# Kernel tuning notes

Hardware: AMD Instinct MI355X
Metric: run time of the kernel (lower is better)

Reference implementation:

```python
import jax, jax.numpy as jnp
import numpy as np
import math

B, S, H = 4, 4096, 64
WINDOW = 2


def setup_inputs() -> dict:
    key = jax.random.key(0)
    ks = jax.random.split(key, 7)
    s = 0.05
    return {
        "feature": jax.random.normal(ks[0], (B, S, H), dtype=jnp.float32),
        "Wq": jax.random.normal(ks[1], (H, H), dtype=jnp.float32) * s,
        "bq": jax.random.normal(ks[2], (H,), dtype=jnp.float32) * s,
        "Wk": jax.random.normal(ks[3], (H, H), dtype=jnp.float32) * s,
        "bk": jax.random.normal(ks[4], (H,), dtype=jnp.float32) * s,
        "Wv": jax.random.normal(ks[5], (H, H), dtype=jnp.float32) * s,
        "bv": jax.random.normal(ks[6], (H,), dtype=jnp.float32) * s,
    }


def reference(feature, Wq, bq, Wk, bk, Wv, bv):
    b, seq, d_k = feature.shape
    # torch nn.Linear: y = x @ W.T + b
    q = feature @ Wq.T + bq  # [B,S,H]
    k = feature @ Wk.T + bk
    v = feature @ Wv.T + bv

    # banded 0/1 mask, |i-j| <= window, then softmax over the FULL row
    # (faithful to the original: zeros outside the band also get exp(0)=1 weight)
    idx = jnp.arange(seq)
    band = (jnp.abs(idx[:, None] - idx[None, :]) <= WINDOW).astype(jnp.float32)  # [S,S]
    weights = jax.nn.softmax(band, axis=-1)  # [S,S]

    # locally-averaged K: weights @ k, shared across batch
    mixed_k = jnp.einsum('st,bth->bsh', weights, k)  # [B,S,H]
    scores = jnp.einsum('bsh,bth->bst', q, mixed_k) / math.sqrt(d_k)  # [B,S,S]
    attn = jax.nn.softmax(scores, axis=-1)
    out = jnp.einsum('bst,bth->bsh', attn, v)  # [B,S,H]
    return out
```

## Files before the change

### kernel.cpp

```cpp
#include <hip/hip_runtime.h>
#include <hip/hip_bf16.h>
#include <math.h>

#define SEQ 4096
#define HD  64
#define NBATCH 4

#define EM1   1.71828182845904523536f
#define INVD5 (1.0f/(4096.f + 5.f*EM1))
#define INVD4 (1.0f/(4096.f + 4.f*EM1))
#define INVD3 (1.0f/(4096.f + 3.f*EM1))

typedef __attribute__((ext_vector_type(8))) short short8;
typedef __attribute__((ext_vector_type(4))) short short4v;
typedef __attribute__((ext_vector_type(4))) float f32x4;

__device__ __forceinline__ f32x4 mfma16(short8 a, short8 b, f32x4 c) {
    return __builtin_amdgcn_mfma_f32_16x16x32_bf16(a, b, c, 0, 0, 0);
}

__device__ __forceinline__ short bfs(float x) {
    __hip_bfloat16 h = __float2bfloat16(x);
    return *(short*)&h;
}

__device__ __forceinline__ float sf(short s) {
    __hip_bfloat16 h;
    *(short*)&h = s;
    return __bfloat162float(h);
}

__device__ __forceinline__ short8 pack8(float4 a, float4 b) {
    short8 r;
    r[0] = bfs(a.x); r[1] = bfs(a.y); r[2] = bfs(a.z); r[3] = bfs(a.w);
    r[4] = bfs(b.x); r[5] = bfs(b.y); r[6] = bfs(b.z); r[7] = bfs(b.w);
    return r;
}

__device__ __forceinline__ float b2f(__hip_bfloat16 h) { return __bfloat162float(h); }

#define WSTR 72

__global__ __launch_bounds__(256, 2) void projm_kernel(
    const float* __restrict__ feat,
    const float* __restrict__ Wq, const float* __restrict__ Wk,
    const float* __restrict__ Wv,
    const float* __restrict__ bq, const float* __restrict__ bk,
    const float* __restrict__ bv,
    __hip_bfloat16* __restrict__ qsb, float* __restrict__ kpart,
    float* __restrict__ vpart, __hip_bfloat16* __restrict__ Mpart,
    float* __restrict__ kedge)
{
    __shared__ __hip_bfloat16 WbL[3 * 64 * WSTR];
    __shared__ __hip_bfloat16 kT[64 * 40];
    __shared__ __hip_bfloat16 vT[64 * 40];
    __shared__ __hip_bfloat16 lvt[64 * 40];
    __shared__ float kred[2][64];
    __shared__ float vred[2][64];

    const int tid  = threadIdx.x;
    const int wv   = tid >> 6, lane = tid & 63;
    const int rh   = wv & 1;
    const int grp  = wv >> 1;
    const int quad = lane >> 4, ln = lane & 15;
    const int R0 = blockIdx.x * 32;
    const int b  = R0 >> 12;
    const int t0 = R0 & (SEQ - 1);
    const int chunk = blockIdx.x & 127;

    short8 af0, af1;
    {
        const float* fp = feat + (size_t)(R0 + rh * 16 + ln) * HD + quad * 8;
        af0 = pack8(*(const float4*)(fp),      *(const float4*)(fp + 4));
        af1 = pack8(*(const float4*)(fp + 32), *(const float4*)(fp + 36));
    }

    short8 hf0, hf1;
    const bool hflag = (rh == 0) ? (t0 > 0) : (t0 < SEQ - 32);
    if (grp == 1) {
        const int hrow = (rh == 0) ? (t0 - 2 + ln) : (t0 + 32 + ln);
        if (ln < 2 && hflag) {
            const float* fp = feat + ((size_t)(b << 12) + hrow) * HD + quad * 8;
            hf0 = pack8(*(const float4*)(fp),      *(const float4*)(fp + 4));
            hf1 = pack8(*(const float4*)(fp + 32), *(const float4*)(fp + 36));
        } else {
            #pragma unroll
            for (int j = 0; j < 8; ++j) { hf0[j] = 0; hf1[j] = 0; }
        }
    }

    {
        const int r = tid >> 2, c = (tid & 3) * 16;
        #pragma unroll
        for (int m = 0; m < 3; ++m) {
            const float* W = (m == 0) ? Wq : (m == 1) ? Wk : Wv;
            const float s = (m == 0) ? 0.125f : 1.f;
            const float* src = W + r * 64 + c;
            float4 a0 = *(const float4*)(src);
            float4 a1 = *(const float4*)(src + 4);
            float4 a2 = *(const float4*)(src + 8);
            float4 a3 = *(const float4*)(src + 12);
            a0.x*=s; a0.y*=s; a0.z*=s; a0.w*=s;
            a1.x*=s; a1.y*=s; a1.z*=s; a1.w*=s;
            a2.x*=s; a2.y*=s; a2.z*=s; a2.w*=s;
            a3.x*=s; a3.y*=s; a3.z*=s; a3.w*=s;
            __hip_bfloat16* dst = WbL + m * 64 * WSTR + r * WSTR + c;
            *(short8*)(dst)     = pack8(a0, a1);
            *(short8*)(dst + 8) = pack8(a2, a3);
        }
    }
    __syncthreads();

    if (grp == 0) {
        #pragma unroll
        for (int ct = 0; ct < 4; ++ct) {
            const int col = ct * 16 + ln;
            {
                const __hip_bfloat16* wp = WbL + col * WSTR + quad * 8;
                short8 b0 = *(const short8*)(wp);
                short8 b1 = *(const short8*)(wp + 32);
                f32x4 c = {};
                c = mfma16(af0, b0, c);
                c = mfma16(af1, b1, c);
                const float bl = bq[col] * 0.125f;
                #pragma unroll
                for (int rr = 0; rr < 4; ++rr)
                    qsb[(size_t)(R0 + rh * 16 + quad * 4 + rr) * HD + col] =
                        __float2bfloat16(c[rr] + bl);
            }
            {
                const __hip_bfloat16* wp = WbL + 64 * WSTR + col * WSTR + quad * 8;
                short8 b0 = *(const short8*)(wp);
                short8 b1 = *(const short8*)(wp + 32);
                f32x4 c = {};
                c = mfma16(af0, b0, c);
                c = mfma16(af1, b1, c);
                float tot = c[0] + c[1] + c[2] + c[3];
                tot += __shfl_xor(tot, 16);
                tot += __shfl_xor(tot, 32);
                if (quad == 0) kred[rh][col] = tot;
                const float bl = bk[col];
                #pragma unroll
                for (int rr = 0; rr < 4; ++rr)
                    kT[col * 40 + rh * 16 + quad * 4 + rr] =
                        __float2bfloat16(c[rr] + bl);
            }
        }
    } else {
        #pragma unroll
        for (int ct = 0; ct < 4; ++ct) {
            const int col = ct * 16 + ln;
            const __hip_bfloat16* wp = WbL + 2 * 64 * WSTR + col * WSTR + quad * 8;
            short8 b0 = *(const short8*)(wp);
            short8 b1 = *(const short8*)(wp + 32);
            f32x4 c = {};
            c = mfma16(af0, b0, c);
            c = mfma16(af1, b1, c);
            float tot = c[0] + c[1] + c[2] + c[3];
            tot += __shfl_xor(tot, 16);
            tot += __shfl_xor(tot, 32);
            if (quad == 0) vred[rh][col] = tot;
            const float bl = bv[col];
            #pragma unroll
            for (int rr = 0; rr < 4; ++rr)
                vT[col * 40 + 2 + rh * 16 + quad * 4 + rr] =
                    __float2bfloat16(c[rr] + bl);
            f32x4 hc = {};
            hc = mfma16(hf0, b0, hc);
            hc = mfma16(hf1, b1, hc);
            if (quad == 0) {
                const int base = (rh == 0) ? 0 : 34;
                vT[col * 40 + base]     = __float2bfloat16(hflag ? hc[0] + bl : 0.f);
                vT[col * 40 + base + 1] = __float2bfloat16(hflag ? hc[1] + bl : 0.f);
            }
        }
    }
    __syncthreads();

    if (tid < 64) {
        kpart[(size_t)blockIdx.x * 64 + tid] =
            kred[0][tid] + kred[1][tid] + 32.f * bk[tid];
        vpart[(size_t)blockIdx.x * 64 + tid] =
            vred[0][tid] + vred[1][tid] + 32.f * bv[tid];
    }

    {
        const int h = tid & 63;
        const int tb = (tid >> 6) * 8;
        short4v u0 = *(const short4v*)&vT[h * 40 + tb];
        short4v u1 = *(const short4v*)&vT[h * 40 + tb + 4];
        short4v u2 = *(const short4v*)&vT[h * 40 + tb + 8];
        float w[12];
        #pragma unroll
        for (int j = 0; j < 4; ++j) {
            w[j]     = sf(u0[j]);
            w[j + 4] = sf(u1[j]);
            w[j + 8] = sf(u2[j]);
        }
        #pragma unroll
        for (int i = 0; i < 8; ++i)
            lvt[h * 40 + tb + i] =
                __float2bfloat16(w[i] + w[i+1] + w[i+2] + w[i+3] + w[i+4]);
    }

    if (chunk == 0) {
        const int t = tid >> 6, h = tid & 63;
        kedge[b * 512 + t * 64 + h] = b2f(kT[h * 40 + t]);
    } else if (chunk == 127) {
        const int t = tid >> 6, h = tid & 63;
        kedge[b * 512 + (4 + t) * 64 + h] = b2f(kT[h * 40 + 28 + t]);
    }
    __syncthreads();

    __hip_bfloat16* mp = Mpart + (size_t)(b * 128 + chunk) * 4096;
    {
        short8 a = *(const short8*)&kT[(wv * 16 + ln) * 40 + quad * 8];
        #pragma unroll
        for (int ct = 0; ct < 4; ++ct) {
            short8 bb = *(const short8*)&lvt[(ct * 16 + ln) * 40 + quad * 8];
            f32x4 acc = {};
            acc = mfma16(a, bb, acc);
            #pragma unroll
            for (int rr = 0; rr < 4; ++rr)
                mp[(wv * 16 + quad * 4 + rr) * 64 + ct * 16 + ln] =
                    __float2bfloat16(acc[rr]);
        }
    }
}

__global__ __launch_bounds__(256) void redprep_kernel(
    const __hip_bfloat16* __restrict__ Mpart, const float* __restrict__ kpart,
    const float* __restrict__ vpart, const float* __restrict__ kedge,
    __hip_bfloat16* __restrict__ MTm, float* __restrict__ mktotF,
    float* __restrict__ ktotF, float* __restrict__ VDs,
    float* __restrict__ VtotF)
{
    const int b = blockIdx.y, x = blockIdx.x;
    const int tid = threadIdx.x;

    if (x < 32) {
        __shared__ float part[16][132];
        const int gl = tid >> 4;
        const int s  = tid & 15;
        const int e  = x * 128 + gl * 8;
        const __hip_bfloat16* src =
            Mpart + ((size_t)b * 128 + s * 8) * 4096 + e;
        float sum[8] = {0.f,0.f,0.f,0.f,0.f,0.f,0.f,0.f};
        #pragma unroll
        for (int c = 0; c < 8; ++c) {
            short8 v = *(const short8*)(src + (size_t)c * 4096);
            #pragma unroll
            for (int j = 0; j < 8; ++j) sum[j] += sf(v[j]);
        }
        #pragma unroll
        for (int j = 0; j < 8; ++j) part[s][gl * 8 + j] = sum[j];
        __syncthreads();
        if (tid < 128) {
            float t = 0.f;
            #pragma unroll
            for (int ss = 0; ss < 16; ++ss) t += part[ss][tid];
            const int e2 = x * 128 + tid;
            const int h1 = e2 >> 6, h2 = e2 & 63;
            MTm[(size_t)b * 4096 + h2 * 64 + h1] =
                __float2bfloat16((EM1 * INVD5) * t);
        }
        return;
    }

    __shared__ float red[4][64];
    __shared__ float red2[4][64];
    const int g = tid >> 6, h2 = tid & 63;
    {
        float kp = 0.f, vp = 0.f;
        for (int j = 0; j < 32; ++j) {
            kp += kpart[(size_t)(b * 128 + g * 32 + j) * 64 + h2];
            vp += vpart[(size_t)(b * 128 + g * 32 + j) * 64 + h2];
        }
        red[g][h2] = kp;
        red2[g][h2] = vp;
    }
    __syncthreads();
    if (tid < 64) {
        const int hh = tid;
        const float kt = red[0][hh] + red[1][hh] + red[2][hh] + red[3][hh];
        const float vt = red2[0][hh] + red2[1][hh] + red2[2][hh] + red2[3][hh];
        const float e0 = kedge[b * 512 + 0 * 64 + hh];
        const float e1 = kedge[b * 512 + 1 * 64 + hh];
        const float e2 = kedge[b * 512 + 2 * 64 + hh];
        const float e3 = kedge[b * 512 + 3 * 64 + hh];
        const float f0 = kedge[b * 512 + 4 * 64 + hh];
        const float f1 = kedge[b * 512 + 5 * 64 + hh];
        const float f2 = kedge[b * 512 + 6 * 64 + hh];
        const float f3 = kedge[b * 512 + 7 * 64 + hh];
        const float Sint = 5.f*kt - 4.f*e0 - 3.f*e1 - 2.f*e2 - e3
                         - f0 - 2.f*f1 - 3.f*f2 - 4.f*f3;
        const float SlocD = Sint * INVD5
                          + (e0+e1+e2 + f1+f2+f3) * INVD3
                          + (e0+e1+e2+e3 + f0+f1+f2+f3) * INVD4;
        mktotF[b * 64 + hh] = kt * (4092.f*INVD5 + 2.f*INVD4 + 2.f*INVD3) + EM1 * SlocD;
        ktotF[b * 64 + hh]  = kt;
        VDs[b * 64 + hh]    = INVD5 * vt;
        VtotF[b * 64 + hh]  = vt;
    }
}

__global__ __launch_bounds__(128) void out_kernel(
    const __hip_bfloat16* __restrict__ qsb, const __hip_bfloat16* __restrict__ MTm,
    const float* __restrict__ mktotF, const float* __restrict__ ktotF,
    const float* __restrict__ VDs, const float* __restrict__ VtotF,
    float* __restrict__ out)
{
    const int tid = threadIdx.x;
    const int wv = tid >> 6, lane = tid & 63;
    const int quad = lane >> 4, ln = lane & 15;
    const int R0 = blockIdx.x * 16;
    const int b = R0 >> 12;

    short8 qa0, qa1;
    {
        const __hip_bfloat16* qp = qsb + (size_t)(R0 + ln) * HD + quad * 8;
        qa0 = *(const short8*)qp;
        qa1 = *(const short8*)(qp + 32);
    }

    const __hip_bfloat16* mtb = MTm + (size_t)b * 4096;
    f32x4 acc[2];
    #pragma unroll
    for (int i = 0; i < 2; ++i) {
        const int ct = wv * 2 + i;
        short8 b0 = *(const short8*)(mtb + (ct * 16 + ln) * 64 + quad * 8);
        short8 b1 = *(const short8*)(mtb + (ct * 16 + ln) * 64 + 32 + quad * 8);
        f32x4 c = {};
        c = mfma16(qa0, b0, c);
        c = mfma16(qa1, b1, c);
        acc[i] = c;
    }

    short8 mk0, mk1, kt0, kt1;
    #pragma unroll
    for (int j = 0; j < 8; ++j) {
        mk0[j] = bfs(mktotF[b * 64 + quad * 8 + j]);
        mk1[j] = bfs(mktotF[b * 64 + 32 + quad * 8 + j]);
        kt0[j] = bfs(ktotF[b * 64 + quad * 8 + j]);
        kt1[j] = bfs(ktotF[b * 64 + 32 + quad * 8 + j]);
    }
    f32x4 accd = {}, acck = {};
    accd = mfma16(qa0, mk0, accd);
    accd = mfma16(qa1, mk1, accd);
    acck = mfma16(qa0, kt0, acck);
    acck = mfma16(qa1, kt1, acck);

    float vt[2], vd[2];
    #pragma unroll
    for (int i = 0; i < 2; ++i) {
        const int ct = wv * 2 + i;
        vt[i] = VtotF[b * 64 + ct * 16 + ln];
        vd[i] = VDs[b * 64 + ct * 16 + ln];
    }

    float inv[4];
    #pragma unroll
    for (int r = 0; r < 4; ++r) inv[r] = 1.f / (4096.f + accd[r]);

    #pragma unroll
    for (int i = 0; i < 2; ++i)
        #pragma unroll
        for (int r = 0; r < 4; ++r)
            out[(size_t)(R0 + quad * 4 + r) * HD + (wv * 2 + i) * 16 + ln] =
                (vt[i] + acc[i][r] + acck[r] * vd[i]) * inv[r];
}

extern "C" void kernel_launch(void* const* d_in, const int* in_sizes, int n_in,
                              void* d_out, int out_size, void* d_ws, size_t ws_size,
                              hipStream_t stream)
{
    const float* feat = (const float*)d_in[0];
    const float* Wq = (const float*)d_in[1];
    const float* bq = (const float*)d_in[2];
    const float* Wk = (const float*)d_in[3];
    const float* bk = (const float*)d_in[4];
    const float* Wv = (const float*)d_in[5];
    const float* bv = (const float*)d_in[6];
    float* out = (float*)d_out;

    char* ws = (char*)d_ws;
    __hip_bfloat16* qsb    = (__hip_bfloat16*)(ws + 0);
    __hip_bfloat16* Mpart  = (__hip_bfloat16*)(ws + (2u << 20));
    float*          kpart  = (float*)(ws + (6u << 20));
    float*          vpart  = (float*)(ws + (6u << 20) + 131072);
    float*          kedge  = (float*)(ws + (6u << 20) + 262144);
    __hip_bfloat16* MTm    = (__hip_bfloat16*)(ws + (6u << 20) + 270336);
    float*          mktotF = (float*)(ws + (6u << 20) + 303104);
    float*          ktotF  = (float*)(ws + (6u << 20) + 304128);
    float*          VDs    = (float*)(ws + (6u << 20) + 305152);
    float*          VtotF  = (float*)(ws + (6u << 20) + 306176);

    projm_kernel<<<dim3(512), dim3(256), 0, stream>>>(
        feat, Wq, Wk, Wv, bq, bk, bv, qsb, kpart, vpart, Mpart, kedge);
    redprep_kernel<<<dim3(33, NBATCH), dim3(256), 0, stream>>>(
        Mpart, kpart, vpart, kedge, MTm, mktotF, ktotF, VDs, VtotF);
    out_kernel<<<dim3(1024), dim3(128), 0, stream>>>(
        qsb, MTm, mktotF, ktotF, VDs, VtotF, out);
}
```

Measured before the change: 79.43 us.

## Fuse three kernels into one cooperative kernel with grid-wide syncs

Merges the projection, reduction/prep and output kernels into one cooperative launch of 512 blocks separated by two grid.sync barriers. The goal is to remove two kernel launch gaps and inter-kernel drain and ramp time. The reduction is redistributed across all 512 blocks, and the output stage now covers 32 rows per block. The trade-off is grid-barrier cost and the requirement that all 512 blocks be co-resident, which the launch bounds of 2 blocks per CU should permit.

```diff
diff --git a/kernel.cpp b/kernel.cpp
--- a/kernel.cpp
+++ b/kernel.cpp
@@ -1,6 +1,9 @@
 #include <hip/hip_runtime.h>
 #include <hip/hip_bf16.h>
+#include <hip/hip_cooperative_groups.h>
 #include <math.h>
+
+namespace cg = cooperative_groups;
 
 #define SEQ 4096
 #define HD  64
@@ -41,7 +44,7 @@
 
 #define WSTR 72
 
-__global__ __launch_bounds__(256, 2) void projm_kernel(
+__global__ __launch_bounds__(256, 2) void fused_kernel(
     const float* __restrict__ feat,
     const float* __restrict__ Wq, const float* __restrict__ Wk,
     const float* __restrict__ Wv,
@@ -49,7 +52,10 @@
     const float* __restrict__ bv,
     __hip_bfloat16* __restrict__ qsb, float* __restrict__ kpart,
     float* __restrict__ vpart, __hip_bfloat16* __restrict__ Mpart,
-    float* __restrict__ kedge)
+    float* __restrict__ kedge,
+    __hip_bfloat16* __restrict__ MTm, float* __restrict__ mktotF,
+    float* __restrict__ ktotF, float* __restrict__ VDs,
+    float* __restrict__ VtotF, float* __restrict__ out)
 {
     __shared__ __hip_bfloat16 WbL[3 * 64 * WSTR];
     __shared__ __hip_bfloat16 kT[64 * 40];
@@ -57,6 +63,11 @@
     __shared__ __hip_bfloat16 lvt[64 * 40];
     __shared__ float kred[2][64];
     __shared__ float vred[2][64];
+    __shared__ float part[8][33];
+    __shared__ float red[4][64];
+    __shared__ float red2[4][64];
+
+    cg::grid_group grid = cg::this_grid();
 
     const int tid  = threadIdx.x;
     const int wv   = tid >> 6, lane = tid & 63;
@@ -212,8 +223,8 @@
     }
     __syncthreads();
 
-    __hip_bfloat16* mp = Mpart + (size_t)(b * 128 + chunk) * 4096;
-    {
+    {
+        __hip_bfloat16* mp = Mpart + (size_t)(b * 128 + chunk) * 4096;
         short8 a = *(const short8*)&kT[(wv * 16 + ln) * 40 + quad * 8];
         #pragma unroll
         for (int ct = 0; ct < 4; ++ct) {
@@ -226,148 +237,136 @@
                     __float2bfloat16(acc[rr]);
         }
     }
-}
-
-__global__ __launch_bounds__(256) void redprep_kernel(
-    const __hip_bfloat16* __restrict__ Mpart, const float* __restrict__ kpart,
-    const float* __restrict__ vpart, const float* __restrict__ kedge,
-    __hip_bfloat16* __restrict__ MTm, float* __restrict__ mktotF,
-    float* __restrict__ ktotF, float* __restrict__ VDs,
-    float* __restrict__ VtotF)
-{
-    const int b = blockIdx.y, x = blockIdx.x;
-    const int tid = threadIdx.x;
-
-    if (x < 32) {
-        __shared__ float part[16][132];
-        const int gl = tid >> 4;
-        const int s  = tid & 15;
-        const int e  = x * 128 + gl * 8;
-        const __hip_bfloat16* src =
-            Mpart + ((size_t)b * 128 + s * 8) * 4096 + e;
-        float sum[8] = {0.f,0.f,0.f,0.f,0.f,0.f,0.f,0.f};
-        #pragma unroll
-        for (int c = 0; c < 8; ++c) {
-            short8 v = *(const short8*)(src + (size_t)c * 4096);
+
+    __threadfence();
+    grid.sync();
+
+    {
+        const int bid = blockIdx.x;
+        if (bid < 4) {
+            const int bb = bid;
+            const int g = tid >> 6, hh = tid & 63;
+            float kp = 0.f, vp = 0.f;
+            for (int j = 0; j < 32; ++j) {
+                kp += kpart[(size_t)(bb * 128 + g * 32 + j) * 64 + hh];
+                vp += vpart[(size_t)(bb * 128 + g * 32 + j) * 64 + hh];
+            }
+            red[g][hh] = kp;
+            red2[g][hh] = vp;
+            __syncthreads();
+            if (tid < 64) {
+                const int h = tid;
+                const float kt = red[0][h] + red[1][h] + red[2][h] + red[3][h];
+                const float vt = red2[0][h] + red2[1][h] + red2[2][h] + red2[3][h];
+                const float e0 = kedge[bb * 512 + 0 * 64 + h];
+                const float e1 = kedge[bb * 512 + 1 * 64 + h];
+                const float e2 = kedge[bb * 512 + 2 * 64 + h];
+                const float e3 = kedge[bb * 512 + 3 * 64 + h];
+                const float f0 = kedge[bb * 512 + 4 * 64 + h];
+                const float f1 = kedge[bb * 512 + 5 * 64 + h];
+                const float f2 = kedge[bb * 512 + 6 * 64 + h];
+                const float f3 = kedge[bb * 512 + 7 * 64 + h];
+                const float Sint = 5.f*kt - 4.f*e0 - 3.f*e1 - 2.f*e2 - e3
+                                 - f0 - 2.f*f1 - 3.f*f2 - 4.f*f3;
+                const float SlocD = Sint * INVD5
+                                  + (e0+e1+e2 + f1+f2+f3) * INVD3
+                                  + (e0+e1+e2+e3 + f0+f1+f2+f3) * INVD4;
+                mktotF[bb * 64 + h] = kt * (4092.f*INVD5 + 2.f*INVD4 + 2.f*INVD3)
+                                    + EM1 * SlocD;
+                ktotF[bb * 64 + h]  = kt;
+                VDs[bb * 64 + h]    = INVD5 * vt;
+                VtotF[bb * 64 + h]  = vt;
+            }
+            __syncthreads();
+        }
+        {
+            const int bb = bid & 3, x = bid >> 2;
+            const int g = tid >> 5, e = tid & 31;
+            const int E = x * 32 + e;
+            const __hip_bfloat16* src =
+                Mpart + ((size_t)bb * 128 + g * 16) * 4096 + E;
+            float s = 0.f;
             #pragma unroll
-            for (int j = 0; j < 8; ++j) sum[j] += sf(v[j]);
-        }
-        #pragma unroll
-        for (int j = 0; j < 8; ++j) part[s][gl * 8 + j] = sum[j];
-        __syncthreads();
-        if (tid < 128) {
-            float t = 0.f;
+            for (int c = 0; c < 16; ++c) s += b2f(src[(size_t)c * 4096]);
+            part[g][e] = s;
+            __syncthreads();
+            if (tid < 32) {
+                float t = 0.f;
+                #pragma unroll
+                for (int g2 = 0; g2 < 8; ++g2) t += part[g2][tid];
+                const int E2 = x * 32 + tid;
+                const int h1 = E2 >> 6, h2 = E2 & 63;
+                MTm[(size_t)bb * 4096 + h2 * 64 + h1] =
+                    __float2bfloat16((EM1 * INVD5) * t);
+            }
+        }
+    }
+
+    __threadfence();
+    grid.sync();
+
+    {
+        const int sub = tid >> 7;
+        const int t2  = tid & 127;
+        const int w3  = t2 >> 6;
+        const int l3  = t2 & 63;
+        const int q3  = l3 >> 4, n3 = l3 & 15;
+        const int R0o = blockIdx.x * 32 + sub * 16;
+        const int b3  = R0o >> 12;
+
+        short8 qa0, qa1;
+        {
+            const __hip_bfloat16* qp = qsb + (size_t)(R0o + n3) * HD + q3 * 8;
+            qa0 = *(const short8*)qp;
+            qa1 = *(const short8*)(qp + 32);
+        }
+
+        const __hip_bfloat16* mtb = MTm + (size_t)b3 * 4096;
+        f32x4 acc[2];
+        #pragma unroll
+        for (int i = 0; i < 2; ++i) {
+            const int ct = w3 * 2 + i;
+            short8 b0 = *(const short8*)(mtb + (ct * 16 + n3) * 64 + q3 * 8);
+            short8 b1 = *(const short8*)(mtb + (ct * 16 + n3) * 64 + 32 + q3 * 8);
+            f32x4 c = {};
+            c = mfma16(qa0, b0, c);
+            c = mfma16(qa1, b1, c);
+            acc[i] = c;
+        }
+
+        short8 mk0, mk1, kt0, kt1;
+        #pragma unroll
+        for (int j = 0; j < 8; ++j) {
+            mk0[j] = bfs(mktotF[b3 * 64 + q3 * 8 + j]);
+            mk1[j] = bfs(mktotF[b3 * 64 + 32 + q3 * 8 + j]);
+            kt0[j] = bfs(ktotF[b3 * 64 + q3 * 8 + j]);
+            kt1[j] = bfs(ktotF[b3 * 64 + 32 + q3 * 8 + j]);
+        }
+        f32x4 accd = {}, acck = {};
+        accd = mfma16(qa0, mk0, accd);
+        accd = mfma16(qa1, mk1, accd);
+        acck = mfma16(qa0, kt0, acck);
+        acck = mfma16(qa1, kt1, acck);
+
+        float vt[2], vd[2];
+        #pragma unroll
+        for (int i = 0; i < 2; ++i) {
+            const int ct = w3 * 2 + i;
+            vt[i] = VtotF[b3 * 64 + ct * 16 + n3];
+            vd[i] = VDs[b3 * 64 + ct * 16 + n3];
+        }
+
+        float inv[4];
+        #pragma unroll
+        for (int r = 0; r < 4; ++r) inv[r] = 1.f / (4096.f + accd[r]);
+
+        #pragma unroll
+        for (int i = 0; i < 2; ++i)
             #pragma unroll
-            for (int ss = 0; ss < 16; ++ss) t += part[ss][tid];
-            const int e2 = x * 128 + tid;
-            const int h1 = e2 >> 6, h2 = e2 & 63;
-            MTm[(size_t)b * 4096 + h2 * 64 + h1] =
-                __float2bfloat16((EM1 * INVD5) * t);
-        }
-        return;
-    }
-
-    __shared__ float red[4][64];
-    __shared__ float red2[4][64];
-    const int g = tid >> 6, h2 = tid & 63;
-    {
-        float kp = 0.f, vp = 0.f;
-        for (int j = 0; j < 32; ++j) {
-            kp += kpart[(size_t)(b * 128 + g * 32 + j) * 64 + h2];
-            vp += vpart[(size_t)(b * 128 + g * 32 + j) * 64 + h2];
-        }
-        red[g][h2] = kp;
-        red2[g][h2] = vp;
-    }
-    __syncthreads();
-    if (tid < 64) {
-        const int hh = tid;
-        const float kt = red[0][hh] + red[1][hh] + red[2][hh] + red[3][hh];
-        const float vt = red2[0][hh] + red2[1][hh] + red2[2][hh] + red2[3][hh];
-        const float e0 = kedge[b * 512 + 0 * 64 + hh];
-        const float e1 = kedge[b * 512 + 1 * 64 + hh];
-        const float e2 = kedge[b * 512 + 2 * 64 + hh];
-        const float e3 = kedge[b * 512 + 3 * 64 + hh];
-        const float f0 = kedge[b * 512 + 4 * 64 + hh];
-        const float f1 = kedge[b * 512 + 5 * 64 + hh];
-        const float f2 = kedge[b * 512 + 6 * 64 + hh];
-        const float f3 = kedge[b * 512 + 7 * 64 + hh];
-        const float Sint = 5.f*kt - 4.f*e0 - 3.f*e1 - 2.f*e2 - e3
-                         - f0 - 2.f*f1 - 3.f*f2 - 4.f*f3;
-        const float SlocD = Sint * INVD5
-                          + (e0+e1+e2 + f1+f2+f3) * INVD3
-                          + (e0+e1+e2+e3 + f0+f1+f2+f3) * INVD4;
-        mktotF[b * 64 + hh] = kt * (4092.f*INVD5 + 2.f*INVD4 + 2.f*INVD3) + EM1 * SlocD;
-        ktotF[b * 64 + hh]  = kt;
-        VDs[b * 64 + hh]    = INVD5 * vt;
-        VtotF[b * 64 + hh]  = vt;
-    }
-}
-
-__global__ __launch_bounds__(128) void out_kernel(
-    const __hip_bfloat16* __restrict__ qsb, const __hip_bfloat16* __restrict__ MTm,
-    const float* __restrict__ mktotF, const float* __restrict__ ktotF,
-    const float* __restrict__ VDs, const float* __restrict__ VtotF,
-    float* __restrict__ out)
-{
-    const int tid = threadIdx.x;
-    const int wv = tid >> 6, lane = tid & 63;
-    const int quad = lane >> 4, ln = lane & 15;
-    const int R0 = blockIdx.x * 16;
-    const int b = R0 >> 12;
-
-    short8 qa0, qa1;
-    {
-        const __hip_bfloat16* qp = qsb + (size_t)(R0 + ln) * HD + quad * 8;
-        qa0 = *(const short8*)qp;
-        qa1 = *(const short8*)(qp + 32);
-    }
-
-    const __hip_bfloat16* mtb = MTm + (size_t)b * 4096;
-    f32x4 acc[2];
-    #pragma unroll
-    for (int i = 0; i < 2; ++i) {
-        const int ct = wv * 2 + i;
-        short8 b0 = *(const short8*)(mtb + (ct * 16 + ln) * 64 + quad * 8);
-        short8 b1 = *(const short8*)(mtb + (ct * 16 + ln) * 64 + 32 + quad * 8);
-        f32x4 c = {};
-        c = mfma16(qa0, b0, c);
-        c = mfma16(qa1, b1, c);
-        acc[i] = c;
-    }
-
-    short8 mk0, mk1, kt0, kt1;
-    #pragma unroll
-    for (int j = 0; j < 8; ++j) {
-        mk0[j] = bfs(mktotF[b * 64 + quad * 8 + j]);
-        mk1[j] = bfs(mktotF[b * 64 + 32 + quad * 8 + j]);
-        kt0[j] = bfs(ktotF[b * 64 + quad * 8 + j]);
-        kt1[j] = bfs(ktotF[b * 64 + 32 + quad * 8 + j]);
-    }
-    f32x4 accd = {}, acck = {};
-    accd = mfma16(qa0, mk0, accd);
-    accd = mfma16(qa1, mk1, accd);
-    acck = mfma16(qa0, kt0, acck);
-    acck = mfma16(qa1, kt1, acck);
-
-    float vt[2], vd[2];
-    #pragma unroll
-    for (int i = 0; i < 2; ++i) {
-        const int ct = wv * 2 + i;
-        vt[i] = VtotF[b * 64 + ct * 16 + ln];
-        vd[i] = VDs[b * 64 + ct * 16 + ln];
-    }
-
-    float inv[4];
-    #pragma unroll
-    for (int r = 0; r < 4; ++r) inv[r] = 1.f / (4096.f + accd[r]);
-
-    #pragma unroll
-    for (int i = 0; i < 2; ++i)
-        #pragma unroll
-        for (int r = 0; r < 4; ++r)
-            out[(size_t)(R0 + quad * 4 + r) * HD + (wv * 2 + i) * 16 + ln] =
-                (vt[i] + acc[i][r] + acck[r] * vd[i]) * inv[r];
+            for (int r = 0; r < 4; ++r)
+                out[(size_t)(R0o + q3 * 4 + r) * HD + (w3 * 2 + i) * 16 + n3] =
+                    (vt[i] + acc[i][r] + acck[r] * vd[i]) * inv[r];
+    }
 }
 
 extern "C" void kernel_launch(void* const* d_in, const int* in_sizes, int n_in,
@@ -395,10 +394,13 @@
     float*          VDs    = (float*)(ws + (6u << 20) + 305152);
     float*          VtotF  = (float*)(ws + (6u << 20) + 306176);
 
-    projm_kernel<<<dim3(512), dim3(256), 0, stream>>>(
-        feat, Wq, Wk, Wv, bq, bk, bv, qsb, kpart, vpart, Mpart, kedge);
-    redprep_kernel<<<dim3(33, NBATCH), dim3(256), 0, stream>>>(
-        Mpart, kpart, vpart, kedge, MTm, mktotF, ktotF, VDs, VtotF);
-    out_kernel<<<dim3(1024), dim3(128), 0, stream>>>(
-        qsb, MTm, mktotF, ktotF, VDs, VtotF, out);
-}
+    void* kargs[] = {
+        (void*)&feat, (void*)&Wq, (void*)&Wk, (void*)&Wv,
+        (void*)&bq, (void*)&bk, (void*)&bv,
+        (void*)&qsb, (void*)&kpart, (void*)&vpart, (void*)&Mpart,
+        (void*)&kedge, (void*)&MTm, (void*)&mktotF, (void*)&ktotF,
+        (void*)&VDs, (void*)&VtotF, (void*)&out
+    };
+    hipLaunchCooperativeKernel((void*)fused_kernel, dim3(512), dim3(256),
+                               kargs, 0, stream);
+}
```

Result: slower. 284.6 us (+258.3%).

## Coalesce q and Mpart stores, widen reduction grid, precast totals to bf16

Applied to the files above, without the earlier changes.

Q projection results are staged in shared memory and written to global memory as 16-byte rows instead of scattered 2-byte stores. Mpart partial products are stored in MFMA fragment order as contiguous 8-byte vectors, and the reduction kernel undoes that permutation when it writes MTm. The reduction grid grows from 33 to 129 blocks per batch, with each block summing a smaller slice. The mk/kt totals are stored as bf16 so out_kernel loads them as vectors instead of converting scalar floats per lane. This trades extra index arithmetic and a small shared buffer for fewer, wider memory transactions and more parallelism in the reduction.

```diff
diff --git a/kernel.cpp b/kernel.cpp
--- a/kernel.cpp
+++ b/kernel.cpp
@@ -40,6 +40,7 @@
 __device__ __forceinline__ float b2f(__hip_bfloat16 h) { return __bfloat162float(h); }
 
 #define WSTR 72
+#define QSTR 72
 
 __global__ __launch_bounds__(256, 2) void projm_kernel(
     const float* __restrict__ feat,
@@ -55,6 +56,7 @@
     __shared__ __hip_bfloat16 kT[64 * 40];
     __shared__ __hip_bfloat16 vT[64 * 40];
     __shared__ __hip_bfloat16 lvt[64 * 40];
+    __shared__ __hip_bfloat16 qR[32 * QSTR];
     __shared__ float kred[2][64];
     __shared__ float vred[2][64];
 
@@ -125,7 +127,7 @@
                 const float bl = bq[col] * 0.125f;
                 #pragma unroll
                 for (int rr = 0; rr < 4; ++rr)
-                    qsb[(size_t)(R0 + rh * 16 + quad * 4 + rr) * HD + col] =
+                    qR[(rh * 16 + quad * 4 + rr) * QSTR + col] =
                         __float2bfloat16(c[rr] + bl);
             }
             {
@@ -177,6 +179,12 @@
     }
     __syncthreads();
 
+    {
+        const int row = tid >> 3, c8 = tid & 7;
+        short8 v = *(const short8*)&qR[row * QSTR + c8 * 8];
+        *(short8*)(qsb + (size_t)(R0 + row) * HD + c8 * 8) = v;
+    }
+
     if (tid < 64) {
         kpart[(size_t)blockIdx.x * 64 + tid] =
             kred[0][tid] + kred[1][tid] + 32.f * bk[tid];
@@ -212,18 +220,18 @@
     }
     __syncthreads();
 
-    __hip_bfloat16* mp = Mpart + (size_t)(b * 128 + chunk) * 4096;
-    {
+    {
+        short4v* mpv = (short4v*)(Mpart + (size_t)(b * 128 + chunk) * 4096);
         short8 a = *(const short8*)&kT[(wv * 16 + ln) * 40 + quad * 8];
         #pragma unroll
         for (int ct = 0; ct < 4; ++ct) {
             short8 bb = *(const short8*)&lvt[(ct * 16 + ln) * 40 + quad * 8];
             f32x4 acc = {};
             acc = mfma16(a, bb, acc);
-            #pragma unroll
-            for (int rr = 0; rr < 4; ++rr)
-                mp[(wv * 16 + quad * 4 + rr) * 64 + ct * 16 + ln] =
-                    __float2bfloat16(acc[rr]);
+            short4v pv;
+            pv[0] = bfs(acc[0]); pv[1] = bfs(acc[1]);
+            pv[2] = bfs(acc[2]); pv[3] = bfs(acc[3]);
+            mpv[(wv * 4 + ct) * 64 + lane] = pv;
         }
     }
 }
@@ -231,36 +239,39 @@
 __global__ __launch_bounds__(256) void redprep_kernel(
     const __hip_bfloat16* __restrict__ Mpart, const float* __restrict__ kpart,
     const float* __restrict__ vpart, const float* __restrict__ kedge,
-    __hip_bfloat16* __restrict__ MTm, float* __restrict__ mktotF,
-    float* __restrict__ ktotF, float* __restrict__ VDs,
-    float* __restrict__ VtotF)
+    __hip_bfloat16* __restrict__ MTm, float* __restrict__ VDs,
+    float* __restrict__ VtotF, __hip_bfloat16* __restrict__ mktotB,
+    __hip_bfloat16* __restrict__ ktotB)
 {
     const int b = blockIdx.y, x = blockIdx.x;
     const int tid = threadIdx.x;
 
-    if (x < 32) {
-        __shared__ float part[16][132];
-        const int gl = tid >> 4;
-        const int s  = tid & 15;
-        const int e  = x * 128 + gl * 8;
+    if (x < 128) {
+        __shared__ float part[32][33];
+        const int cg = tid >> 3;
+        const int eg = tid & 7;
         const __hip_bfloat16* src =
-            Mpart + ((size_t)b * 128 + s * 8) * 4096 + e;
-        float sum[8] = {0.f,0.f,0.f,0.f,0.f,0.f,0.f,0.f};
-        #pragma unroll
-        for (int c = 0; c < 8; ++c) {
-            short8 v = *(const short8*)(src + (size_t)c * 4096);
-            #pragma unroll
-            for (int j = 0; j < 8; ++j) sum[j] += sf(v[j]);
-        }
-        #pragma unroll
-        for (int j = 0; j < 8; ++j) part[s][gl * 8 + j] = sum[j];
+            Mpart + ((size_t)b * 128 + cg * 4) * 4096 + x * 32 + eg * 4;
+        float s0 = 0.f, s1 = 0.f, s2 = 0.f, s3 = 0.f;
+        #pragma unroll
+        for (int c = 0; c < 4; ++c) {
+            short4v v = *(const short4v*)(src + (size_t)c * 4096);
+            s0 += sf(v[0]); s1 += sf(v[1]); s2 += sf(v[2]); s3 += sf(v[3]);
+        }
+        part[cg][eg * 4 + 0] = s0;
+        part[cg][eg * 4 + 1] = s1;
+        part[cg][eg * 4 + 2] = s2;
+        part[cg][eg * 4 + 3] = s3;
         __syncthreads();
-        if (tid < 128) {
+        if (tid < 32) {
             float t = 0.f;
             #pragma unroll
-            for (int ss = 0; ss < 16; ++ss) t += part[ss][tid];
-            const int e2 = x * 128 + tid;
-            const int h1 = e2 >> 6, h2 = e2 & 63;
+            for (int g = 0; g < 32; ++g) t += part[g][tid];
+            const int E  = x * 32 + tid;
+            const int rr = E & 3, l = (E >> 2) & 63;
+            const int ct = (E >> 8) & 3, w = (E >> 10) & 3;
+            const int h1 = w * 16 + (l >> 4) * 4 + rr;
+            const int h2 = ct * 16 + (l & 15);
             MTm[(size_t)b * 4096 + h2 * 64 + h1] =
                 __float2bfloat16((EM1 * INVD5) * t);
         }
@@ -297,8 +308,9 @@
         const float SlocD = Sint * INVD5
                           + (e0+e1+e2 + f1+f2+f3) * INVD3
                           + (e0+e1+e2+e3 + f0+f1+f2+f3) * INVD4;
-        mktotF[b * 64 + hh] = kt * (4092.f*INVD5 + 2.f*INVD4 + 2.f*INVD3) + EM1 * SlocD;
-        ktotF[b * 64 + hh]  = kt;
+        const float mk = kt * (4092.f*INVD5 + 2.f*INVD4 + 2.f*INVD3) + EM1 * SlocD;
+        mktotB[b * 64 + hh] = __float2bfloat16(mk);
+        ktotB[b * 64 + hh]  = __float2bfloat16(kt);
         VDs[b * 64 + hh]    = INVD5 * vt;
         VtotF[b * 64 + hh]  = vt;
     }
@@ -306,7 +318,7 @@
 
 __global__ __launch_bounds__(128) void out_kernel(
     const __hip_bfloat16* __restrict__ qsb, const __hip_bfloat16* __restrict__ MTm,
-    const float* __restrict__ mktotF, const float* __restrict__ ktotF,
+    const __hip_bfloat16* __restrict__ mktotB, const __hip_bfloat16* __restrict__ ktotB,
     const float* __restrict__ VDs, const float* __restrict__ VtotF,
     float* __restrict__ out)
 {
@@ -336,14 +348,11 @@
         acc[i] = c;
     }
 
-    short8 mk0, mk1, kt0, kt1;
-    #pragma unroll
-    for (int j = 0; j < 8; ++j) {
-        mk0[j] = bfs(mktotF[b * 64 + quad * 8 + j]);
-        mk1[j] = bfs(mktotF[b * 64 + 32 + quad * 8 + j]);
-        kt0[j] = bfs(ktotF[b * 64 + quad * 8 + j]);
-        kt1[j] = bfs(ktotF[b * 64 + 32 + quad * 8 + j]);
-    }
+    short8 mk0 = *(const short8*)(mktotB + b * 64 + quad * 8);
+    short8 mk1 = *(const short8*)(mktotB + b * 64 + 32 + quad * 8);
+    short8 kt0 = *(const short8*)(ktotB + b * 64 + quad * 8);
+    short8 kt1 = *(const short8*)(ktotB + b * 64 + 32 + quad * 8);
+
     f32x4 accd = {}, acck = {};
     accd = mfma16(qa0, mk0, accd);
     accd = mfma16(qa1, mk1, accd);
@@ -390,15 +399,15 @@
     float*          vpart  = (float*)(ws + (6u << 20) + 131072);
     float*          kedge  = (float*)(ws + (6u << 20) + 262144);
     __hip_bfloat16* MTm    = (__hip_bfloat16*)(ws + (6u << 20) + 270336);
-    float*          mktotF = (float*)(ws + (6u << 20) + 303104);
-    float*          ktotF  = (float*)(ws + (6u << 20) + 304128);
-    float*          VDs    = (float*)(ws + (6u << 20) + 305152);
-    float*          VtotF  = (float*)(ws + (6u << 20) + 306176);
+    float*          VDs    = (float*)(ws + (6u << 20) + 303104);
+    float*          VtotF  = (float*)(ws + (6u << 20) + 304128);
+    __hip_bfloat16* mktotB = (__hip_bfloat16*)(ws + (6u << 20) + 305152);
+    __hip_bfloat16* ktotB  = (__hip_bfloat16*)(ws + (6u << 20) + 305664);
 
     projm_kernel<<<dim3(512), dim3(256), 0, stream>>>(
         feat, Wq, Wk, Wv, bq, bk, bv, qsb, kpart, vpart, Mpart, kedge);
-    redprep_kernel<<<dim3(33, NBATCH), dim3(256), 0, stream>>>(
-        Mpart, kpart, vpart, kedge, MTm, mktotF, ktotF, VDs, VtotF);
+    redprep_kernel<<<dim3(129, NBATCH), dim3(256), 0, stream>>>(
+        Mpart, kpart, vpart, kedge, MTm, VDs, VtotF, mktotB, ktotB);
     out_kernel<<<dim3(1024), dim3(128), 0, stream>>>(
-        qsb, MTm, mktotF, ktotF, VDs, VtotF, out);
-}
+        qsb, MTm, mktotB, ktotB, VDs, VtotF, out);
+}
```

New measurement: 81.43 us. 2.5% more time.

## Replace partial-sum buffers and reduction kernel with global float atomics

Applied to the files above, without the earlier changes.

The projection kernel now accumulates the per-chunk 64x64 K^T·localV products and the K/V column totals straight into per-batch fp32 buffers with unsafeAtomicAdd, instead of writing bf16 partials for a separate reduction kernel. The small per-batch prep (mk, kt, vd, vt) moves into the output kernel's prologue and is shared through LDS, and the output kernel scales and converts the fp32 M matrix to bf16 on load. This drops one kernel launch and about 4 MB of partial-buffer traffic. In exchange it adds a memset, heavy atomic contention (128 chunks per batch adding into the same 4096 floats), and redundant prep work in every output block.

```diff
diff --git a/kernel.cpp b/kernel.cpp
--- a/kernel.cpp
+++ b/kernel.cpp
@@ -34,6 +34,13 @@
     short8 r;
     r[0] = bfs(a.x); r[1] = bfs(a.y); r[2] = bfs(a.z); r[3] = bfs(a.w);
     r[4] = bfs(b.x); r[5] = bfs(b.y); r[6] = bfs(b.z); r[7] = bfs(b.w);
+    return r;
+}
+
+__device__ __forceinline__ short8 pack8s(float4 a, float4 b, float s) {
+    short8 r;
+    r[0] = bfs(a.x*s); r[1] = bfs(a.y*s); r[2] = bfs(a.z*s); r[3] = bfs(a.w*s);
+    r[4] = bfs(b.x*s); r[5] = bfs(b.y*s); r[6] = bfs(b.z*s); r[7] = bfs(b.w*s);
     return r;
 }
 
@@ -47,8 +54,8 @@
     const float* __restrict__ Wv,
     const float* __restrict__ bq, const float* __restrict__ bk,
     const float* __restrict__ bv,
-    __hip_bfloat16* __restrict__ qsb, float* __restrict__ kpart,
-    float* __restrict__ vpart, __hip_bfloat16* __restrict__ Mpart,
+    __hip_bfloat16* __restrict__ qsb, float* __restrict__ MTf,
+    float* __restrict__ ktotF, float* __restrict__ VtotF,
     float* __restrict__ kedge)
 {
     __shared__ __hip_bfloat16 WbL[3 * 64 * WSTR];
@@ -178,10 +185,10 @@
     __syncthreads();
 
     if (tid < 64) {
-        kpart[(size_t)blockIdx.x * 64 + tid] =
-            kred[0][tid] + kred[1][tid] + 32.f * bk[tid];
-        vpart[(size_t)blockIdx.x * 64 + tid] =
-            vred[0][tid] + vred[1][tid] + 32.f * bv[tid];
+        unsafeAtomicAdd(&ktotF[b * 64 + tid],
+                        kred[0][tid] + kred[1][tid] + 32.f * bk[tid]);
+        unsafeAtomicAdd(&VtotF[b * 64 + tid],
+                        vred[0][tid] + vred[1][tid] + 32.f * bv[tid]);
     }
 
     {
@@ -212,8 +219,8 @@
     }
     __syncthreads();
 
-    __hip_bfloat16* mp = Mpart + (size_t)(b * 128 + chunk) * 4096;
-    {
+    {
+        float* mt = MTf + (size_t)b * 4096;
         short8 a = *(const short8*)&kT[(wv * 16 + ln) * 40 + quad * 8];
         #pragma unroll
         for (int ct = 0; ct < 4; ++ct) {
@@ -222,68 +229,32 @@
             acc = mfma16(a, bb, acc);
             #pragma unroll
             for (int rr = 0; rr < 4; ++rr)
-                mp[(wv * 16 + quad * 4 + rr) * 64 + ct * 16 + ln] =
-                    __float2bfloat16(acc[rr]);
-        }
-    }
-}
-
-__global__ __launch_bounds__(256) void redprep_kernel(
-    const __hip_bfloat16* __restrict__ Mpart, const float* __restrict__ kpart,
-    const float* __restrict__ vpart, const float* __restrict__ kedge,
-    __hip_bfloat16* __restrict__ MTm, float* __restrict__ mktotF,
-    float* __restrict__ ktotF, float* __restrict__ VDs,
-    float* __restrict__ VtotF)
+                unsafeAtomicAdd(
+                    &mt[(ct * 16 + ln) * 64 + wv * 16 + quad * 4 + rr], acc[rr]);
+        }
+    }
+}
+
+__global__ __launch_bounds__(128) void out_kernel(
+    const __hip_bfloat16* __restrict__ qsb, const float* __restrict__ MTf,
+    const float* __restrict__ ktotF, const float* __restrict__ VtotF,
+    const float* __restrict__ kedge, float* __restrict__ out)
 {
-    const int b = blockIdx.y, x = blockIdx.x;
+    __shared__ __align__(16) __hip_bfloat16 mkB[64];
+    __shared__ __align__(16) __hip_bfloat16 ktB[64];
+    __shared__ float vdL[64];
+    __shared__ float vtL[64];
+
     const int tid = threadIdx.x;
-
-    if (x < 32) {
-        __shared__ float part[16][132];
-        const int gl = tid >> 4;
-        const int s  = tid & 15;
-        const int e  = x * 128 + gl * 8;
-        const __hip_bfloat16* src =
-            Mpart + ((size_t)b * 128 + s * 8) * 4096 + e;
-        float sum[8] = {0.f,0.f,0.f,0.f,0.f,0.f,0.f,0.f};
-        #pragma unroll
-        for (int c = 0; c < 8; ++c) {
-            short8 v = *(const short8*)(src + (size_t)c * 4096);
-            #pragma unroll
-            for (int j = 0; j < 8; ++j) sum[j] += sf(v[j]);
-        }
-        #pragma unroll
-        for (int j = 0; j < 8; ++j) part[s][gl * 8 + j] = sum[j];
-        __syncthreads();
-        if (tid < 128) {
-            float t = 0.f;
-            #pragma unroll
-            for (int ss = 0; ss < 16; ++ss) t += part[ss][tid];
-            const int e2 = x * 128 + tid;
-            const int h1 = e2 >> 6, h2 = e2 & 63;
-            MTm[(size_t)b * 4096 + h2 * 64 + h1] =
-                __float2bfloat16((EM1 * INVD5) * t);
-        }
-        return;
-    }
-
-    __shared__ float red[4][64];
-    __shared__ float red2[4][64];
-    const int g = tid >> 6, h2 = tid & 63;
-    {
-        float kp = 0.f, vp = 0.f;
-        for (int j = 0; j < 32; ++j) {
-            kp += kpart[(size_t)(b * 128 + g * 32 + j) * 64 + h2];
-            vp += vpart[(size_t)(b * 128 + g * 32 + j) * 64 + h2];
-        }
-        red[g][h2] = kp;
-        red2[g][h2] = vp;
-    }
-    __syncthreads();
+    const int wv = tid >> 6, lane = tid & 63;
+    const int quad = lane >> 4, ln = lane & 15;
+    const int R0 = blockIdx.x * 16;
+    const int b = R0 >> 12;
+
     if (tid < 64) {
         const int hh = tid;
-        const float kt = red[0][hh] + red[1][hh] + red[2][hh] + red[3][hh];
-        const float vt = red2[0][hh] + red2[1][hh] + red2[2][hh] + red2[3][hh];
+        const float kt = ktotF[b * 64 + hh];
+        const float vt = VtotF[b * 64 + hh];
         const float e0 = kedge[b * 512 + 0 * 64 + hh];
         const float e1 = kedge[b * 512 + 1 * 64 + hh];
         const float e2 = kedge[b * 512 + 2 * 64 + hh];
@@ -297,24 +268,12 @@
         const float SlocD = Sint * INVD5
                           + (e0+e1+e2 + f1+f2+f3) * INVD3
                           + (e0+e1+e2+e3 + f0+f1+f2+f3) * INVD4;
-        mktotF[b * 64 + hh] = kt * (4092.f*INVD5 + 2.f*INVD4 + 2.f*INVD3) + EM1 * SlocD;
-        ktotF[b * 64 + hh]  = kt;
-        VDs[b * 64 + hh]    = INVD5 * vt;
-        VtotF[b * 64 + hh]  = vt;
-    }
-}
-
-__global__ __launch_bounds__(128) void out_kernel(
-    const __hip_bfloat16* __restrict__ qsb, const __hip_bfloat16* __restrict__ MTm,
-    const float* __restrict__ mktotF, const float* __restrict__ ktotF,
-    const float* __restrict__ VDs, const float* __restrict__ VtotF,
-    float* __restrict__ out)
-{
-    const int tid = threadIdx.x;
-    const int wv = tid >> 6, lane = tid & 63;
-    const int quad = lane >> 4, ln = lane & 15;
-    const int R0 = blockIdx.x * 16;
-    const int b = R0 >> 12;
+        const float mk = kt * (4092.f*INVD5 + 2.f*INVD4 + 2.f*INVD3) + EM1 * SlocD;
+        mkB[hh] = __float2bfloat16(mk);
+        ktB[hh] = __float2bfloat16(kt);
+        vdL[hh] = INVD5 * vt;
+        vtL[hh] = vt;
+    }
 
     short8 qa0, qa1;
     {
@@ -323,27 +282,30 @@
         qa1 = *(const short8*)(qp + 32);
     }
 
-    const __hip_bfloat16* mtb = MTm + (size_t)b * 4096;
+    const float SC = EM1 * INVD5;
+    const float* mtb = MTf + (size_t)b * 4096;
     f32x4 acc[2];
     #pragma unroll
     for (int i = 0; i < 2; ++i) {
         const int ct = wv * 2 + i;
-        short8 b0 = *(const short8*)(mtb + (ct * 16 + ln) * 64 + quad * 8);
-        short8 b1 = *(const short8*)(mtb + (ct * 16 + ln) * 64 + 32 + quad * 8);
+        const float* mrow = mtb + (ct * 16 + ln) * 64;
+        short8 b0 = pack8s(*(const float4*)(mrow + quad * 8),
+                           *(const float4*)(mrow + quad * 8 + 4), SC);
+        short8 b1 = pack8s(*(const float4*)(mrow + 32 + quad * 8),
+                           *(const float4*)(mrow + 36 + quad * 8), SC);
         f32x4 c = {};
         c = mfma16(qa0, b0, c);
         c = mfma16(qa1, b1, c);
         acc[i] = c;
     }
 
-    short8 mk0, mk1, kt0, kt1;
-    #pragma unroll
-    for (int j = 0; j < 8; ++j) {
-        mk0[j] = bfs(mktotF[b * 64 + quad * 8 + j]);
-        mk1[j] = bfs(mktotF[b * 64 + 32 + quad * 8 + j]);
-        kt0[j] = bfs(ktotF[b * 64 + quad * 8 + j]);
-        kt1[j] = bfs(ktotF[b * 64 + 32 + quad * 8 + j]);
-    }
+    __syncthreads();
+
+    short8 mk0 = *(const short8*)&mkB[quad * 8];
+    short8 mk1 = *(const short8*)&mkB[32 + quad * 8];
+    short8 kt0 = *(const short8*)&ktB[quad * 8];
+    short8 kt1 = *(const short8*)&ktB[32 + quad * 8];
+
     f32x4 accd = {}, acck = {};
     accd = mfma16(qa0, mk0, accd);
     accd = mfma16(qa1, mk1, accd);
@@ -354,8 +316,8 @@
     #pragma unroll
     for (int i = 0; i < 2; ++i) {
         const int ct = wv * 2 + i;
-        vt[i] = VtotF[b * 64 + ct * 16 + ln];
-        vd[i] = VDs[b * 64 + ct * 16 + ln];
+        vt[i] = vtL[ct * 16 + ln];
+        vd[i] = vdL[ct * 16 + ln];
     }
 
     float inv[4];
@@ -384,21 +346,16 @@
     float* out = (float*)d_out;
 
     char* ws = (char*)d_ws;
-    __hip_bfloat16* qsb    = (__hip_bfloat16*)(ws + 0);
-    __hip_bfloat16* Mpart  = (__hip_bfloat16*)(ws + (2u << 20));
-    float*          kpart  = (float*)(ws + (6u << 20));
-    float*          vpart  = (float*)(ws + (6u << 20) + 131072);
-    float*          kedge  = (float*)(ws + (6u << 20) + 262144);
-    __hip_bfloat16* MTm    = (__hip_bfloat16*)(ws + (6u << 20) + 270336);
-    float*          mktotF = (float*)(ws + (6u << 20) + 303104);
-    float*          ktotF  = (float*)(ws + (6u << 20) + 304128);
-    float*          VDs    = (float*)(ws + (6u << 20) + 305152);
-    float*          VtotF  = (float*)(ws + (6u << 20) + 306176);
+    __hip_bfloat16* qsb   = (__hip_bfloat16*)(ws + 0);
+    float*          MTf   = (float*)(ws + (2u << 20));
+    float*          ktotF = (float*)(ws + (2u << 20) + 65536);
+    float*          VtotF = (float*)(ws + (2u << 20) + 66560);
+    float*          kedge = (float*)(ws + (2u << 20) + 67584);
+
+    hipMemsetAsync(ws + (2u << 20), 0, 67584, stream);
 
     projm_kernel<<<dim3(512), dim3(256), 0, stream>>>(
-        feat, Wq, Wk, Wv, bq, bk, bv, qsb, kpart, vpart, Mpart, kedge);
-    redprep_kernel<<<dim3(33, NBATCH), dim3(256), 0, stream>>>(
-        Mpart, kpart, vpart, kedge, MTm, mktotF, ktotF, VDs, VtotF);
+        feat, Wq, Wk, Wv, bq, bk, bv, qsb, MTf, ktotF, VtotF, kedge);
     out_kernel<<<dim3(1024), dim3(128), 0, stream>>>(
-        qsb, MTm, mktotF, ktotF, VDs, VtotF, out);
-}
+        qsb, MTf, ktotF, VtotF, kedge, out);
+}
```

Measured after the change: 116.4 us. +46.6%, slower.
